# Performance work log

Measured on AMD Instinct MI355X. Metric: run time of the kernel, lower is better.

## Reference

```python
import jax, jax.numpy as jnp
import numpy as np

B, S, H = 4, 512, 128
ALIGN_STRENGTH = 1.0


def setup_inputs() -> dict:
    key = jax.random.key(0)
    ks = jax.random.split(key, 12)
    s2h = 1.0 / np.sqrt(2 * H)
    sh = 1.0 / np.sqrt(H)
    return {
        "x": jax.random.normal(ks[0], (B, S, H), dtype=jnp.float32),
        "ref_seq": jax.random.normal(ks[1], (B, S, H), dtype=jnp.float32),
        # alignment_scoring: Linear(2H,H) split into Wa (acts on seq1) and Wb (acts on seq2)
        "Wa": jax.random.normal(ks[2], (H, H), dtype=jnp.float32) * s2h,
        "Wb": jax.random.normal(ks[3], (H, H), dtype=jnp.float32) * s2h,
        "b1": jnp.zeros((H,), dtype=jnp.float32),
        "W2": jax.random.normal(ks[4], (H, 1), dtype=jnp.float32) * sh,
        "b2": jnp.zeros((1,), dtype=jnp.float32),
        # path_predictor: Linear(H,H) -> ReLU -> Linear(H,3) -> LogSoftmax
        "Wp1": jax.random.normal(ks[5], (H, H), dtype=jnp.float32) * sh,
        "bp1": jnp.zeros((H,), dtype=jnp.float32),
        "Wp2": jax.random.normal(ks[6], (H, 3), dtype=jnp.float32) * sh,
        "bp2": jnp.zeros((3,), dtype=jnp.float32),
    }


def _forward(x, ref_seq, Wa, Wb, b1, W2, b2, Wp1, bp1, Wp2, bp2):
    # alignment matrix A[b,i,j] = sigmoid(MLP([x_i ; ref_j]))  -- concat-Linear
    # expressed as split matmuls to avoid materializing the [B,S,S,2H] concat.
    a = jnp.einsum("bsh,hk->bsk", x, Wa)            # [B,S,H]
    c = jnp.einsum("bsh,hk->bsk", ref_seq, Wb)      # [B,S,H]
    hdn = jax.nn.relu(a[:, :, None, :] + c[:, None, :, :] + b1)  # [B,S,S,H]
    A = jax.nn.sigmoid(jnp.einsum("bijh,ho->bijo", hdn, W2)[..., 0] + b2[0])  # [B,S,S]

    # path_logits: LogSoftmax(Linear(ReLU(Linear(x))))
    P = jax.nn.log_softmax(jax.nn.relu(x @ Wp1 + bp1) @ Wp2 + bp2, axis=-1)  # [B,S,3]

    idx = jnp.arange(S)
    diag = A[:, idx, idx]                       # A[t,t], [B,S]
    t = idx[1:]
    match_s = diag[:, 1:] * P[:, 1:, 0]          # A[t,t]   * P[t,0]
    insert_s = A[:, t - 1, t] * P[:, 1:, 1]      # A[t-1,t] * P[t,1]
    delete_s = A[:, t, t - 1] * P[:, 1:, 2]      # A[t,t-1] * P[t,2]
    scores = jnp.stack([match_s, insert_s, delete_s], axis=-1)  # [B,S-1,3]
    op = jnp.argmax(scores, axis=-1)             # first-max tiebreak like Python max

    alpha = (ALIGN_STRENGTH * diag[:, 1:])[..., None]            # [B,S-1,1]
    match_out = (1.0 - alpha) * x[:, 1:] + alpha * ref_seq[:, 1:]
    insert_out = ref_seq[:, 1:]                  # best_idx+1 == t (< S always)
    delete_out = x[:, :-1]                       # x[t-1]

    op_e = op[..., None]
    tail = jnp.where(op_e == 0, match_out, jnp.where(op_e == 1, insert_out, delete_out))
    return jnp.concatenate([x[:, :1], tail], axis=1)  # aligned[0] = x[0]


def reference(x, ref_seq, Wa, Wb, b1, W2, b2, Wp1, bp1, Wp2, bp2):
    return _forward(x, ref_seq, Wa, Wb, b1, W2, b2, Wp1, bp1, Wp2, bp2)
```

## Files before the change

### kernel.cpp

```cpp
#include <hip/hip_runtime.h>
#include <math.h>

namespace {
constexpr int Bn = 4;
constexpr int Sn = 512;
constexpr int Hn = 128;
constexpr int ROWS = 8;
constexpr int NBLK = Bn * (Sn / ROWS);
constexpr int NGRP = 4;
constexpr int NTHR = NGRP * 128;
constexpr int HCHUNK = Hn / NGRP;
constexpr int NACC = 2 * (ROWS + 1) + ROWS;

__device__ inline float wave_sum(float v) {
    v += __shfl_xor(v, 32);
    v += __shfl_xor(v, 16);
    v += __shfl_xor(v, 8);
    v += __shfl_xor(v, 4);
    v += __shfl_xor(v, 2);
    v += __shfl_xor(v, 1);
    return v;
}
}

__global__ __launch_bounds__(NTHR) void tsa_kernel(
    const float* __restrict__ x,   const float* __restrict__ ref,
    const float* __restrict__ Wa,  const float* __restrict__ Wb,
    const float* __restrict__ b1,  const float* __restrict__ W2,
    const float* __restrict__ b2,  const float* __restrict__ Wp1,
    const float* __restrict__ bp1, const float* __restrict__ Wp2,
    const float* __restrict__ bp2, float* __restrict__ out)
{
    const int tid = threadIdx.x;
    const int k   = tid & 127;
    const int grp = tid >> 7;
    const int b   = blockIdx.x >> 6;
    const int t0  = (blockIdx.x & 63) * ROWS;

    const float* xbase = x   + (size_t)b * Sn * Hn;
    const float* rbase = ref + (size_t)b * Sn * Hn;

    const int g0 = (t0 == 0) ? 0 : (t0 - 1);

    __shared__ float xs[(ROWS + 1) * Hn];
    __shared__ float rs[(ROWS + 1) * Hn];
    __shared__ float pacc[NACC * NTHR];
    __shared__ float alphaA[ROWS];
    __shared__ int   opA[ROWS];

    for (int idx = tid; idx < (ROWS + 1) * (Hn / 4); idx += NTHR) {
        const int row = idx >> 5;
        const int c4  = idx & 31;
        const int g   = (row == 0) ? g0 : (t0 - 1 + row);
        ((float4*)xs)[row * 32 + c4] = *(const float4*)(xbase + (size_t)g * Hn + c4 * 4);
        ((float4*)rs)[row * 32 + c4] = *(const float4*)(rbase + (size_t)g * Hn + c4 * 4);
    }
    __syncthreads();

    float aa[ROWS + 1], cc[ROWS + 1], hp[ROWS];
#pragma unroll
    for (int i = 0; i <= ROWS; ++i) { aa[i] = 0.f; cc[i] = 0.f; }
#pragma unroll
    for (int j = 0; j < ROWS; ++j) hp[j] = 0.f;

    const int hbase = grp * HCHUNK;
#pragma unroll
    for (int h2 = 0; h2 < HCHUNK; h2 += 4) {
        const int h = hbase + h2;
        float wa[4], wb[4], wp[4];
#pragma unroll
        for (int u = 0; u < 4; ++u) {
            wa[u] = Wa[(h + u) * Hn + k];
            wb[u] = Wb[(h + u) * Hn + k];
            wp[u] = Wp1[(h + u) * Hn + k];
        }
#pragma unroll
        for (int i = 0; i <= ROWS; ++i) {
            const float4 xv = *(const float4*)(xs + i * Hn + h);
            const float4 rv = *(const float4*)(rs + i * Hn + h);
            aa[i] += xv.x * wa[0]; aa[i] += xv.y * wa[1];
            aa[i] += xv.z * wa[2]; aa[i] += xv.w * wa[3];
            cc[i] += rv.x * wb[0]; cc[i] += rv.y * wb[1];
            cc[i] += rv.z * wb[2]; cc[i] += rv.w * wb[3];
            if (i >= 1) {
                hp[i-1] += xv.x * wp[0]; hp[i-1] += xv.y * wp[1];
                hp[i-1] += xv.z * wp[2]; hp[i-1] += xv.w * wp[3];
            }
        }
    }

#pragma unroll
    for (int i = 0; i <= ROWS; ++i) {
        pacc[i * NTHR + grp * 128 + k]              = aa[i];
        pacc[(ROWS + 1 + i) * NTHR + grp * 128 + k] = cc[i];
    }
#pragma unroll
    for (int j = 0; j < ROWS; ++j)
        pacc[(2 * (ROWS + 1) + j) * NTHR + grp * 128 + k] = hp[j];
    __syncthreads();

    for (int idx = tid; idx < NACC * 128; idx += NTHR) {
        const int i = idx >> 7, kk = idx & 127;
        float s = 0.f;
#pragma unroll
        for (int g = 0; g < NGRP; ++g) s += pacc[i * NTHR + g * 128 + kk];
        pacc[i * NTHR + kk] = s;
    }
    __syncthreads();

    {
        const int j  = tid >> 6;
        const int ln = tid & 63;
        float vm = 0.f, vi = 0.f, vd = 0.f, l0 = 0.f, l1 = 0.f, l2 = 0.f;
#pragma unroll
        for (int half = 0; half < 2; ++half) {
            const int kk = ln + 64 * half;
            const float at   = pacc[(j + 1) * NTHR + kk];
            const float atm1 = pacc[j * NTHR + kk];
            const float ct   = pacc[(ROWS + 1 + j + 1) * NTHR + kk];
            const float ctm1 = pacc[(ROWS + 1 + j) * NTHR + kk];
            const float hvp  = pacc[(2 * (ROWS + 1) + j) * NTHR + kk];
            const float b1k = b1[kk], w2k = W2[kk], bp1k = bp1[kk];
            vm += fmaxf(at   + ct   + b1k, 0.f) * w2k;
            vi += fmaxf(atm1 + ct   + b1k, 0.f) * w2k;
            vd += fmaxf(at   + ctm1 + b1k, 0.f) * w2k;
            const float hv = fmaxf(hvp + bp1k, 0.f);
            l0 += hv * Wp2[kk * 3 + 0];
            l1 += hv * Wp2[kk * 3 + 1];
            l2 += hv * Wp2[kk * 3 + 2];
        }
        vm = wave_sum(vm); vi = wave_sum(vi); vd = wave_sum(vd);
        l0 = wave_sum(l0); l1 = wave_sum(l1); l2 = wave_sum(l2);
        if (ln == 0) {
            const float b2v = b2[0];
            const float Am = 1.f / (1.f + expf(-(vm + b2v)));
            const float Ai = 1.f / (1.f + expf(-(vi + b2v)));
            const float Ad = 1.f / (1.f + expf(-(vd + b2v)));
            float q0 = l0 + bp2[0], q1 = l1 + bp2[1], q2 = l2 + bp2[2];
            const float mx  = fmaxf(q0, fmaxf(q1, q2));
            const float lse = mx + logf(expf(q0 - mx) + expf(q1 - mx) + expf(q2 - mx));
            const float s0 = Am * (q0 - lse);
            const float s1 = Ai * (q1 - lse);
            const float s2 = Ad * (q2 - lse);
            int op = 0; float best = s0;
            if (s1 > best) { op = 1; best = s1; }
            if (s2 > best) { op = 2; }
            opA[j]    = op;
            alphaA[j] = Am;
        }
    }
    __syncthreads();

    for (int e = tid; e < ROWS * 128; e += NTHR) {
        const int j  = e >> 7;
        const int kk = e & 127;
        const int t  = t0 + j;
        float o;
        if (t == 0) {
            o = xs[1 * Hn + kk];
        } else {
            const int   op = opA[j];
            const float al = alphaA[j];
            const float xt   = xs[(j + 1) * Hn + kk];
            const float rt   = rs[(j + 1) * Hn + kk];
            const float xtm1 = xs[j * Hn + kk];
            if (op == 0)      o = (1.f - al) * xt + al * rt;
            else if (op == 1) o = rt;
            else              o = xtm1;
        }
        out[((size_t)b * Sn + t) * Hn + kk] = o;
    }
}

extern "C" void kernel_launch(void* const* d_in, const int* in_sizes, int n_in,
                              void* d_out, int out_size, void* d_ws, size_t ws_size,
                              hipStream_t stream) {
    const float* x    = (const float*)d_in[0];
    const float* ref  = (const float*)d_in[1];
    const float* Wa   = (const float*)d_in[2];
    const float* Wb   = (const float*)d_in[3];
    const float* b1   = (const float*)d_in[4];
    const float* W2   = (const float*)d_in[5];
    const float* b2   = (const float*)d_in[6];
    const float* Wp1  = (const float*)d_in[7];
    const float* bp1  = (const float*)d_in[8];
    const float* Wp2  = (const float*)d_in[9];
    const float* bp2  = (const float*)d_in[10];
    float* out = (float*)d_out;

    tsa_kernel<<<NBLK, NTHR, 0, stream>>>(x, ref, Wa, Wb, b1, W2, b2,
                                          Wp1, bp1, Wp2, bp2, out);
}
```

Before: 82.51 us.

## Split H reduction across eight waves with two output columns per lane

Each thread now computes two output columns (k and k+64) over a smaller H chunk, using eight groups of 64 threads instead of four groups of 128. Every LDS float4 broadcast of x/ref now feeds twice as many FMAs, which cuts shared-memory reads per FMA. The cross-group reduction uses float4 loads. The cost is twice as many accumulator registers per thread and a larger partial-sum buffer with more groups to reduce. Total threads per block stay at 512.

```diff
diff --git a/kernel.cpp b/kernel.cpp
--- a/kernel.cpp
+++ b/kernel.cpp
@@ -7,8 +7,8 @@
 constexpr int Hn = 128;
 constexpr int ROWS = 8;
 constexpr int NBLK = Bn * (Sn / ROWS);
-constexpr int NGRP = 4;
-constexpr int NTHR = NGRP * 128;
+constexpr int NGRP = 8;
+constexpr int NTHR = NGRP * 64;
 constexpr int HCHUNK = Hn / NGRP;
 constexpr int NACC = 2 * (ROWS + 1) + ROWS;
 
@@ -31,11 +31,13 @@
     const float* __restrict__ bp1, const float* __restrict__ Wp2,
     const float* __restrict__ bp2, float* __restrict__ out)
 {
-    const int tid = threadIdx.x;
-    const int k   = tid & 127;
-    const int grp = tid >> 7;
-    const int b   = blockIdx.x >> 6;
-    const int t0  = (blockIdx.x & 63) * ROWS;
+    const int tid  = threadIdx.x;
+    const int lane = tid & 63;
+    const int grp  = tid >> 6;
+    const int b    = blockIdx.x >> 6;
+    const int t0   = (blockIdx.x & 63) * ROWS;
+    const int k0   = lane;
+    const int k1   = lane + 64;
 
     const float* xbase = x   + (size_t)b * Sn * Hn;
     const float* rbase = ref + (size_t)b * Sn * Hn;
@@ -44,7 +46,7 @@
 
     __shared__ float xs[(ROWS + 1) * Hn];
     __shared__ float rs[(ROWS + 1) * Hn];
-    __shared__ float pacc[NACC * NTHR];
+    __shared__ float pacc[NACC * NGRP * Hn];
     __shared__ float alphaA[ROWS];
     __shared__ int   opA[ROWS];
 
@@ -57,54 +59,68 @@
     }
     __syncthreads();
 
-    float aa[ROWS + 1], cc[ROWS + 1], hp[ROWS];
-#pragma unroll
-    for (int i = 0; i <= ROWS; ++i) { aa[i] = 0.f; cc[i] = 0.f; }
-#pragma unroll
-    for (int j = 0; j < ROWS; ++j) hp[j] = 0.f;
+    float aa[ROWS + 1][2], cc[ROWS + 1][2], hp[ROWS][2];
+#pragma unroll
+    for (int i = 0; i <= ROWS; ++i) { aa[i][0]=0.f; aa[i][1]=0.f; cc[i][0]=0.f; cc[i][1]=0.f; }
+#pragma unroll
+    for (int j = 0; j < ROWS; ++j) { hp[j][0]=0.f; hp[j][1]=0.f; }
 
     const int hbase = grp * HCHUNK;
 #pragma unroll
     for (int h2 = 0; h2 < HCHUNK; h2 += 4) {
         const int h = hbase + h2;
-        float wa[4], wb[4], wp[4];
+        float wa[4][2], wb[4][2], wp[4][2];
 #pragma unroll
         for (int u = 0; u < 4; ++u) {
-            wa[u] = Wa[(h + u) * Hn + k];
-            wb[u] = Wb[(h + u) * Hn + k];
-            wp[u] = Wp1[(h + u) * Hn + k];
+            wa[u][0] = Wa[(h + u) * Hn + k0];  wa[u][1] = Wa[(h + u) * Hn + k1];
+            wb[u][0] = Wb[(h + u) * Hn + k0];  wb[u][1] = Wb[(h + u) * Hn + k1];
+            wp[u][0] = Wp1[(h + u) * Hn + k0]; wp[u][1] = Wp1[(h + u) * Hn + k1];
         }
 #pragma unroll
         for (int i = 0; i <= ROWS; ++i) {
             const float4 xv = *(const float4*)(xs + i * Hn + h);
             const float4 rv = *(const float4*)(rs + i * Hn + h);
-            aa[i] += xv.x * wa[0]; aa[i] += xv.y * wa[1];
-            aa[i] += xv.z * wa[2]; aa[i] += xv.w * wa[3];
-            cc[i] += rv.x * wb[0]; cc[i] += rv.y * wb[1];
-            cc[i] += rv.z * wb[2]; cc[i] += rv.w * wb[3];
+#pragma unroll
+            for (int c = 0; c < 2; ++c) {
+                aa[i][c] += xv.x * wa[0][c]; aa[i][c] += xv.y * wa[1][c];
+                aa[i][c] += xv.z * wa[2][c]; aa[i][c] += xv.w * wa[3][c];
+                cc[i][c] += rv.x * wb[0][c]; cc[i][c] += rv.y * wb[1][c];
+                cc[i][c] += rv.z * wb[2][c]; cc[i][c] += rv.w * wb[3][c];
+            }
             if (i >= 1) {
-                hp[i-1] += xv.x * wp[0]; hp[i-1] += xv.y * wp[1];
-                hp[i-1] += xv.z * wp[2]; hp[i-1] += xv.w * wp[3];
+#pragma unroll
+                for (int c = 0; c < 2; ++c) {
+                    hp[i-1][c] += xv.x * wp[0][c]; hp[i-1][c] += xv.y * wp[1][c];
+                    hp[i-1][c] += xv.z * wp[2][c]; hp[i-1][c] += xv.w * wp[3][c];
+                }
             }
         }
     }
 
 #pragma unroll
     for (int i = 0; i <= ROWS; ++i) {
-        pacc[i * NTHR + grp * 128 + k]              = aa[i];
-        pacc[(ROWS + 1 + i) * NTHR + grp * 128 + k] = cc[i];
-    }
-#pragma unroll
-    for (int j = 0; j < ROWS; ++j)
-        pacc[(2 * (ROWS + 1) + j) * NTHR + grp * 128 + k] = hp[j];
-    __syncthreads();
-
-    for (int idx = tid; idx < NACC * 128; idx += NTHR) {
-        const int i = idx >> 7, kk = idx & 127;
-        float s = 0.f;
-#pragma unroll
-        for (int g = 0; g < NGRP; ++g) s += pacc[i * NTHR + g * 128 + kk];
-        pacc[i * NTHR + kk] = s;
+        pacc[(i * NGRP + grp) * Hn + k0]              = aa[i][0];
+        pacc[(i * NGRP + grp) * Hn + k1]              = aa[i][1];
+        pacc[((ROWS + 1 + i) * NGRP + grp) * Hn + k0] = cc[i][0];
+        pacc[((ROWS + 1 + i) * NGRP + grp) * Hn + k1] = cc[i][1];
+    }
+#pragma unroll
+    for (int j = 0; j < ROWS; ++j) {
+        pacc[((2 * (ROWS + 1) + j) * NGRP + grp) * Hn + k0] = hp[j][0];
+        pacc[((2 * (ROWS + 1) + j) * NGRP + grp) * Hn + k1] = hp[j][1];
+    }
+    __syncthreads();
+
+    for (int idx = tid; idx < NACC * (Hn / 4); idx += NTHR) {
+        const int i  = idx >> 5;
+        const int c4 = idx & 31;
+        float4 s = make_float4(0.f, 0.f, 0.f, 0.f);
+#pragma unroll
+        for (int g = 0; g < NGRP; ++g) {
+            const float4 v = ((const float4*)pacc)[(i * NGRP + g) * (Hn / 4) + c4];
+            s.x += v.x; s.y += v.y; s.z += v.z; s.w += v.w;
+        }
+        ((float4*)pacc)[(i * NGRP) * (Hn / 4) + c4] = s;
     }
     __syncthreads();
 
@@ -115,11 +131,11 @@
 #pragma unroll
         for (int half = 0; half < 2; ++half) {
             const int kk = ln + 64 * half;
-            const float at   = pacc[(j + 1) * NTHR + kk];
-            const float atm1 = pacc[j * NTHR + kk];
-            const float ct   = pacc[(ROWS + 1 + j + 1) * NTHR + kk];
-            const float ctm1 = pacc[(ROWS + 1 + j) * NTHR + kk];
-            const float hvp  = pacc[(2 * (ROWS + 1) + j) * NTHR + kk];
+            const float at   = pacc[(j + 1) * (NGRP * Hn) + kk];
+            const float atm1 = pacc[j * (NGRP * Hn) + kk];
+            const float ct   = pacc[(ROWS + 1 + j + 1) * (NGRP * Hn) + kk];
+            const float ctm1 = pacc[(ROWS + 1 + j) * (NGRP * Hn) + kk];
+            const float hvp  = pacc[(2 * (ROWS + 1) + j) * (NGRP * Hn) + kk];
             const float b1k = b1[kk], w2k = W2[kk], bp1k = bp1[kk];
             vm += fmaxf(at   + ct   + b1k, 0.f) * w2k;
             vi += fmaxf(atm1 + ct   + b1k, 0.f) * w2k;
```

After: 81.93 us. No clear change (-0.7%).
